# Optimization experiments

Hardware: AMD Instinct MI355X
Metric: run time of the kernel (lower is better)

## Reference

```python
import jax, jax.numpy as jnp
import numpy as np

T, B, D_DEC, D_ENC = 2048, 128, 512, 512

def setup_inputs() -> dict:
    key = jax.random.key(0)
    k1, k2, k3, k4 = jax.random.split(key, 4)
    x = jax.random.normal(k1, (B, D_DEC), dtype=jnp.float32)
    encoder_states = jax.random.normal(k2, (T, B, D_ENC), dtype=jnp.float32)
    # nn.Linear(decoder_hidden_size, encoder_hidden_size): W [out,in], b [out]
    W = jax.random.normal(k3, (D_ENC, D_DEC), dtype=jnp.float32) / np.sqrt(D_DEC)
    b = jax.random.normal(k4, (D_ENC,), dtype=jnp.float32) * 0.01
    return {"x": x, "encoder_states": encoder_states, "W": W, "b": b}

def reference(x, encoder_states, W, b):
    # x: [B, D_dec] -> projected query xp: [B, E]
    xp = x @ W.T + b
    # scores[b,t] = sum_e xp[b,e] * enc[t,b,e]  (the Python loop, batched)
    scores = jnp.einsum('be,tbe->bt', xp, encoder_states)
    attn = jax.nn.softmax(scores, axis=1)                 # [B, T]
    context = jnp.einsum('bt,tbe->be', attn, encoder_states)  # [B, E]
    return jnp.concatenate([xp, context], axis=1)         # [B, 2E]
```

## Files before the change

### kernel.cpp

```cpp
#include <hip/hip_runtime.h>
#include <math.h>

#define T_DIM   2048
#define B_DIM   128
#define E_DIM   512
#define NSPLIT  8
#define TC      (T_DIM / NSPLIT)

__device__ __forceinline__ float wave_reduce_sum(float v) {
    v += __shfl_xor(v, 1,  64);
    v += __shfl_xor(v, 2,  64);
    v += __shfl_xor(v, 4,  64);
    v += __shfl_xor(v, 8,  64);
    v += __shfl_xor(v, 16, 64);
    v += __shfl_xor(v, 32, 64);
    return v;
}

__global__ __launch_bounds__(256) void proj_kernel(
    const float* __restrict__ x, const float* __restrict__ W,
    const float* __restrict__ bias, float* __restrict__ xp,
    float* __restrict__ out)
{
    const int b      = blockIdx.x;
    const int echunk = blockIdx.y;
    const int tid    = threadIdx.x;
    const int lane   = tid & 63;
    const int wave   = tid >> 6;

    const float4* x4 = (const float4*)(x + (size_t)b * E_DIM);
    const float4 xq0 = x4[lane];
    const float4 xq1 = x4[64 + lane];

    const int ebase = echunk * 128;
    for (int e = ebase + wave; e < ebase + 128; e += 4) {
        const float4* w4 = (const float4*)(W + (size_t)e * E_DIM);
        const float4 w0 = w4[lane];
        const float4 w1 = w4[64 + lane];
        float p = w0.x*xq0.x + w0.y*xq0.y + w0.z*xq0.z + w0.w*xq0.w;
        p      += w1.x*xq1.x + w1.y*xq1.y + w1.z*xq1.z + w1.w*xq1.w;
        p = wave_reduce_sum(p);
        if (lane == 0) {
            float v = p + bias[e];
            xp[(size_t)b * E_DIM + e] = v;
            out[(size_t)b * (2 * E_DIM) + e] = v;
        }
    }
}

__global__ __launch_bounds__(256) void attn_partial_kernel(
    const float* __restrict__ enc, const float* __restrict__ xp,
    float* __restrict__ m_part, float* __restrict__ l_part,
    float* __restrict__ acc_part)
{
    const int b    = blockIdx.x;
    const int s    = blockIdx.y;
    const int tid  = threadIdx.x;
    const int lane = tid & 63;
    const int wave = tid >> 6;

    const float4* xp4 = (const float4*)(xp + (size_t)b * E_DIM);
    const float4 xq0 = xp4[lane];
    const float4 xq1 = xp4[64 + lane];

    float m = -INFINITY;
    float l = 0.0f;
    float4 a0 = make_float4(0.f, 0.f, 0.f, 0.f);
    float4 a1 = make_float4(0.f, 0.f, 0.f, 0.f);

    const int t0 = s * TC + wave * (TC / 4);
    for (int i = 0; i < TC / 4; ++i) {
        const int t = t0 + i;
        const float4* e4 = (const float4*)(enc + ((size_t)t * B_DIM + b) * E_DIM);
        const float4 e0 = e4[lane];
        const float4 e1 = e4[64 + lane];

        float p = e0.x*xq0.x + e0.y*xq0.y + e0.z*xq0.z + e0.w*xq0.w;
        p      += e1.x*xq1.x + e1.y*xq1.y + e1.z*xq1.z + e1.w*xq1.w;
        p = wave_reduce_sum(p);

        const float m_new = fmaxf(m, p);
        const float scale = __expf(m - m_new);
        const float pt    = __expf(p - m_new);
        l = l * scale + pt;
        a0.x = a0.x * scale + pt * e0.x;
        a0.y = a0.y * scale + pt * e0.y;
        a0.z = a0.z * scale + pt * e0.z;
        a0.w = a0.w * scale + pt * e0.w;
        a1.x = a1.x * scale + pt * e1.x;
        a1.y = a1.y * scale + pt * e1.y;
        a1.z = a1.z * scale + pt * e1.z;
        a1.w = a1.w * scale + pt * e1.w;
        m = m_new;
    }

    __shared__ float lds_m[4];
    __shared__ float lds_l[4];
    __shared__ __align__(16) float lds_acc[4][E_DIM];

    if (lane == 0) lds_m[wave] = m;
    __syncthreads();
    const float M = fmaxf(fmaxf(lds_m[0], lds_m[1]), fmaxf(lds_m[2], lds_m[3]));
    const float wscale = __expf(m - M);

    float4* lacc = (float4*)&lds_acc[wave][0];
    lacc[lane]      = make_float4(a0.x*wscale, a0.y*wscale, a0.z*wscale, a0.w*wscale);
    lacc[64 + lane] = make_float4(a1.x*wscale, a1.y*wscale, a1.z*wscale, a1.w*wscale);
    if (lane == 0) lds_l[wave] = l * wscale;
    __syncthreads();

    const int pid = b * NSPLIT + s;
    if (tid == 0) {
        m_part[pid] = M;
        l_part[pid] = lds_l[0] + lds_l[1] + lds_l[2] + lds_l[3];
    }
    if (tid < 128) {
        float4 sum = make_float4(0.f, 0.f, 0.f, 0.f);
        for (int w = 0; w < 4; ++w) {
            const float4 v = ((const float4*)&lds_acc[w][0])[tid];
            sum.x += v.x; sum.y += v.y; sum.z += v.z; sum.w += v.w;
        }
        ((float4*)(acc_part + (size_t)pid * E_DIM))[tid] = sum;
    }
}

__global__ __launch_bounds__(128) void combine_kernel(
    const float* __restrict__ m_part, const float* __restrict__ l_part,
    const float* __restrict__ acc_part, float* __restrict__ out)
{
    const int b   = blockIdx.x;
    const int tid = threadIdx.x;

    float M = -INFINITY;
    for (int s = 0; s < NSPLIT; ++s) M = fmaxf(M, m_part[b * NSPLIT + s]);
    float w[NSPLIT];
    float L = 0.f;
    for (int s = 0; s < NSPLIT; ++s) {
        w[s] = __expf(m_part[b * NSPLIT + s] - M);
        L += w[s] * l_part[b * NSPLIT + s];
    }
    const float inv = 1.0f / L;

    float4 sum = make_float4(0.f, 0.f, 0.f, 0.f);
    for (int s = 0; s < NSPLIT; ++s) {
        const float4 v = ((const float4*)(acc_part + (size_t)(b * NSPLIT + s) * E_DIM))[tid];
        sum.x += w[s] * v.x; sum.y += w[s] * v.y;
        sum.z += w[s] * v.z; sum.w += w[s] * v.w;
    }
    const float4 r = make_float4(sum.x*inv, sum.y*inv, sum.z*inv, sum.w*inv);
    ((float4*)(out + (size_t)b * (2 * E_DIM) + E_DIM))[tid] = r;
}

extern "C" void kernel_launch(void* const* d_in, const int* in_sizes, int n_in,
                              void* d_out, int out_size, void* d_ws, size_t ws_size,
                              hipStream_t stream) {
    (void)in_sizes; (void)n_in; (void)out_size; (void)ws_size;
    const float* x    = (const float*)d_in[0];
    const float* enc  = (const float*)d_in[1];
    const float* W    = (const float*)d_in[2];
    const float* bias = (const float*)d_in[3];
    float* out = (float*)d_out;

    float* ws       = (float*)d_ws;
    float* xp       = ws;
    float* m_part   = ws + 65536;
    float* l_part   = ws + 66560;
    float* acc_part = ws + 67584;

    proj_kernel<<<dim3(B_DIM, 4), 256, 0, stream>>>(x, W, bias, xp, out);
    attn_partial_kernel<<<dim3(B_DIM, NSPLIT), 256, 0, stream>>>(enc, xp, m_part, l_part, acc_part);
    combine_kernel<<<B_DIM, 128, 0, stream>>>(m_part, l_part, acc_part, out);
}
```

Before: 715.6 us.

## Batch four encoder rows per softmax step and double the T split

The attention partial kernel now loads four encoder rows per iteration and reduces their four dot products together in one float4 shuffle reduction. The online-softmax rescale then runs once per four rows instead of once per row. This exposes more memory-level parallelism and cuts the serial shuffle and exp chain per row. The T split is also raised from 8 to 16, doubling the grid to improve occupancy, and the workspace offsets are resized to fit the larger partial buffers. The costs are higher register pressure and a combine step that reads twice as many partials.

```diff
diff --git a/kernel.cpp b/kernel.cpp
--- a/kernel.cpp
+++ b/kernel.cpp
@@ -4,8 +4,10 @@
 #define T_DIM   2048
 #define B_DIM   128
 #define E_DIM   512
-#define NSPLIT  8
+#define NSPLIT  16
 #define TC      (T_DIM / NSPLIT)
+#define TW      (TC / 4)
+#define ROWS    4
 
 __device__ __forceinline__ float wave_reduce_sum(float v) {
     v += __shfl_xor(v, 1,  64);
@@ -14,6 +16,17 @@
     v += __shfl_xor(v, 8,  64);
     v += __shfl_xor(v, 16, 64);
     v += __shfl_xor(v, 32, 64);
+    return v;
+}
+
+__device__ __forceinline__ float4 wave_reduce_sum4(float4 v) {
+    #pragma unroll
+    for (int mask = 1; mask < 64; mask <<= 1) {
+        v.x += __shfl_xor(v.x, mask, 64);
+        v.y += __shfl_xor(v.y, mask, 64);
+        v.z += __shfl_xor(v.z, mask, 64);
+        v.w += __shfl_xor(v.w, mask, 64);
+    }
     return v;
 }
 
@@ -68,29 +81,49 @@
     float4 a0 = make_float4(0.f, 0.f, 0.f, 0.f);
     float4 a1 = make_float4(0.f, 0.f, 0.f, 0.f);
 
-    const int t0 = s * TC + wave * (TC / 4);
-    for (int i = 0; i < TC / 4; ++i) {
-        const int t = t0 + i;
-        const float4* e4 = (const float4*)(enc + ((size_t)t * B_DIM + b) * E_DIM);
-        const float4 e0 = e4[lane];
-        const float4 e1 = e4[64 + lane];
-
-        float p = e0.x*xq0.x + e0.y*xq0.y + e0.z*xq0.z + e0.w*xq0.w;
-        p      += e1.x*xq1.x + e1.y*xq1.y + e1.z*xq1.z + e1.w*xq1.w;
-        p = wave_reduce_sum(p);
-
-        const float m_new = fmaxf(m, p);
+    const int t0 = s * TC + wave * TW;
+    const size_t row_stride = (size_t)B_DIM * E_DIM;
+    const float* base = enc + ((size_t)t0 * B_DIM + b) * E_DIM;
+
+    #pragma unroll 1
+    for (int i = 0; i < TW; i += ROWS) {
+        float4 e0[ROWS], e1[ROWS];
+        #pragma unroll
+        for (int r = 0; r < ROWS; ++r) {
+            const float4* e4 = (const float4*)(base + (size_t)(i + r) * row_stride);
+            e0[r] = e4[lane];
+            e1[r] = e4[64 + lane];
+        }
+
+        float4 d;
+        {
+            float t[ROWS];
+            #pragma unroll
+            for (int r = 0; r < ROWS; ++r) {
+                t[r]  = e0[r].x*xq0.x + e0[r].y*xq0.y + e0[r].z*xq0.z + e0[r].w*xq0.w;
+                t[r] += e1[r].x*xq1.x + e1[r].y*xq1.y + e1[r].z*xq1.z + e1[r].w*xq1.w;
+            }
+            d = make_float4(t[0], t[1], t[2], t[3]);
+        }
+        d = wave_reduce_sum4(d);
+
+        const float mrow  = fmaxf(fmaxf(d.x, d.y), fmaxf(d.z, d.w));
+        const float m_new = fmaxf(m, mrow);
         const float scale = __expf(m - m_new);
-        const float pt    = __expf(p - m_new);
-        l = l * scale + pt;
-        a0.x = a0.x * scale + pt * e0.x;
-        a0.y = a0.y * scale + pt * e0.y;
-        a0.z = a0.z * scale + pt * e0.z;
-        a0.w = a0.w * scale + pt * e0.w;
-        a1.x = a1.x * scale + pt * e1.x;
-        a1.y = a1.y * scale + pt * e1.y;
-        a1.z = a1.z * scale + pt * e1.z;
-        a1.w = a1.w * scale + pt * e1.w;
+        const float p0 = __expf(d.x - m_new);
+        const float p1 = __expf(d.y - m_new);
+        const float p2 = __expf(d.z - m_new);
+        const float p3 = __expf(d.w - m_new);
+        l = l * scale + (p0 + p1 + p2 + p3);
+
+        a0.x = a0.x*scale + p0*e0[0].x + p1*e0[1].x + p2*e0[2].x + p3*e0[3].x;
+        a0.y = a0.y*scale + p0*e0[0].y + p1*e0[1].y + p2*e0[2].y + p3*e0[3].y;
+        a0.z = a0.z*scale + p0*e0[0].z + p1*e0[1].z + p2*e0[2].z + p3*e0[3].z;
+        a0.w = a0.w*scale + p0*e0[0].w + p1*e0[1].w + p2*e0[2].w + p3*e0[3].w;
+        a1.x = a1.x*scale + p0*e1[0].x + p1*e1[1].x + p2*e1[2].x + p3*e1[3].x;
+        a1.y = a1.y*scale + p0*e1[0].y + p1*e1[1].y + p2*e1[2].y + p3*e1[3].y;
+        a1.z = a1.z*scale + p0*e1[0].z + p1*e1[1].z + p2*e1[2].z + p3*e1[3].z;
+        a1.w = a1.w*scale + p0*e1[0].w + p1*e1[1].w + p2*e1[2].w + p3*e1[3].w;
         m = m_new;
     }
 
@@ -164,8 +197,8 @@
     float* ws       = (float*)d_ws;
     float* xp       = ws;
     float* m_part   = ws + 65536;
-    float* l_part   = ws + 66560;
-    float* acc_part = ws + 67584;
+    float* l_part   = ws + 65536 + 2048;
+    float* acc_part = ws + 65536 + 4096;
 
     proj_kernel<<<dim3(B_DIM, 4), 256, 0, stream>>>(x, W, bias, xp, out);
     attn_partial_kernel<<<dim3(B_DIM, NSPLIT), 256, 0, stream>>>(enc, xp, m_part, l_part, acc_part);
```

New measurement: 713.9 us. About the same (-0.2%).
